# Performance work log

Measured on AMD Instinct MI355X. Metric: run time of the kernel, lower is better.

## Reference

```python
import jax, jax.numpy as jnp
import numpy as np

S, B, I, H, O = 1024, 64, 512, 2048, 512


def setup_inputs() -> dict:
    key = jax.random.key(0)
    k1, k2, k3, k4, k5 = jax.random.split(key, 5)
    X = jax.random.normal(k1, (S, B, I), dtype=jnp.float32)
    W_ih = jax.random.normal(k2, (H, I), dtype=jnp.float32) * (1.0 / np.sqrt(I))
    hh = jax.random.uniform(k3, (H,), dtype=jnp.float32)  # clamped-to-[-1,1] diagonal recurrence
    W_ho = jax.random.normal(k4, (O, H), dtype=jnp.float32) * (1.0 / np.sqrt(H))
    b_ho = jax.random.normal(k5, (O,), dtype=jnp.float32) * 0.01
    return {"X": X, "W_ih": W_ih, "hh": hh, "W_ho": W_ho, "b_ho": b_ho}


def reference(X, W_ih, hh, W_ho, b_ho):
    # Batch the input->hidden projection over the whole sequence in one GEMM:
    # u[s,b,h] = X[s,b,i] @ W_ih[h,i]^T
    u = jnp.einsum('sbi,hi->sbh', X, W_ih)
    h0 = jnp.zeros((X.shape[1], W_ih.shape[0]), dtype=X.dtype)

    def step(h, u_t):
        h_new = jnp.abs(u_t + hh * h)
        return h_new, None

    h_final, _ = jax.lax.scan(step, h0, u)
    Y = h_final @ W_ho.T + b_ho  # [B, O]
    return Y
```

## Files before the change

kernel.cpp:

```cpp
#include <hip/hip_runtime.h>
#include <hip/hip_bf16.h>
#include <stdint.h>

#define S_LEN 1024
#define B_SZ  64
#define I_SZ  512
#define H_SZ  2048
#define O_SZ  512

typedef __bf16  bf16x8 __attribute__((ext_vector_type(8)));
typedef float   f32x4  __attribute__((ext_vector_type(4)));

static __device__ __forceinline__ ushort f2bf(float f) {
  union { float f; unsigned u; } v; v.f = f;
  unsigned r = v.u + 0x7FFFu + ((v.u >> 16) & 1u);
  return (ushort)(r >> 16);
}
static __device__ __forceinline__ float bf2f(ushort u) {
  return __builtin_bit_cast(float, (unsigned)u << 16);
}

#define GLOAD_LDS16(gp, lp) \
  __builtin_amdgcn_global_load_lds( \
      (__attribute__((address_space(1))) void*)(gp), \
      (__attribute__((address_space(3))) void*)(lp), 16, 0, 0)

__global__ __launch_bounds__(256) void convert_f32_bf16_kernel(
    const float4* __restrict__ in, ushort4* __restrict__ out, int n4) {
  int i = blockIdx.x * 256 + threadIdx.x;
  if (i >= n4) return;
  float4 v = in[i];
  ushort4 o; o.x = f2bf(v.x); o.y = f2bf(v.y); o.z = f2bf(v.z); o.w = f2bf(v.w);
  out[i] = o;
}

__global__ __launch_bounds__(256) void convert_x_kernel(
    const float* __restrict__ X, ushort* __restrict__ Xt) {
  const int row  = blockIdx.x * 4 + (threadIdx.x >> 6);
  const int lane = threadIdx.x & 63;
  const int s = row >> 6, b = row & 63;
  const float* src = X + (size_t)row * I_SZ + lane * 8;
  float4 v0 = *(const float4*)src;
  float4 v1 = *(const float4*)(src + 4);
  union { ushort h[8]; uint4 v; } o;
  o.h[0] = f2bf(v0.x); o.h[1] = f2bf(v0.y); o.h[2] = f2bf(v0.z); o.h[3] = f2bf(v0.w);
  o.h[4] = f2bf(v1.x); o.h[5] = f2bf(v1.y); o.h[6] = f2bf(v1.z); o.h[7] = f2bf(v1.w);
  *(uint4*)(Xt + ((size_t)b * S_LEN + s) * I_SZ + lane * 8) = o.v;
}

__global__ __launch_bounds__(256) void init_y_kernel(
    const float* __restrict__ bho, float* __restrict__ Y) {
  int idx = blockIdx.x * 256 + threadIdx.x;
  Y[idx] = bho[idx & (O_SZ - 1)];
}

#define SCAN16(colp, s0_) do { \
    ushort4 v0 = *(const ushort4*)&(colp)[(s0_)]; \
    ushort4 v1 = *(const ushort4*)&(colp)[(s0_) + 4]; \
    ushort4 v2 = *(const ushort4*)&(colp)[(s0_) + 8]; \
    ushort4 v3 = *(const ushort4*)&(colp)[(s0_) + 12]; \
    p = fmaf(c, fabsf(p), bf2f(v0.x)); p = fmaf(c, fabsf(p), bf2f(v0.y)); \
    p = fmaf(c, fabsf(p), bf2f(v0.z)); p = fmaf(c, fabsf(p), bf2f(v0.w)); \
    p = fmaf(c, fabsf(p), bf2f(v1.x)); p = fmaf(c, fabsf(p), bf2f(v1.y)); \
    p = fmaf(c, fabsf(p), bf2f(v1.z)); p = fmaf(c, fabsf(p), bf2f(v1.w)); \
    p = fmaf(c, fabsf(p), bf2f(v2.x)); p = fmaf(c, fabsf(p), bf2f(v2.y)); \
    p = fmaf(c, fabsf(p), bf2f(v2.z)); p = fmaf(c, fabsf(p), bf2f(v2.w)); \
    p = fmaf(c, fabsf(p), bf2f(v3.x)); p = fmaf(c, fabsf(p), bf2f(v3.y)); \
    p = fmaf(c, fabsf(p), bf2f(v3.z)); p = fmaf(c, fabsf(p), bf2f(v3.w)); \
  } while (0)

__global__ __launch_bounds__(256, 3) void fused_gemm_scan_kernel(
    const ushort* __restrict__ Xbf,
    const ushort* __restrict__ Wbf,
    const float* __restrict__ hh,
    const float* __restrict__ Who,
    float* __restrict__ Y) {
  __shared__ __align__(16) ushort smem[16896];
  ushort* As = smem;
  ushort* Bs = smem + 8192;
  ushort* Cs = smem;

  const int tid  = threadIdx.x;
  const int wave = tid >> 6;
  const int lane = tid & 63;

  const int bid = blockIdx.x;
  const int xcd = bid & 7;
  const int g   = bid >> 3;
  const int b   = (xcd << 3) | (g & 7);
  const int ht  = g >> 3;

  const int wm = (wave >> 1) * 64;
  const int wn = (wave & 1) * 64;
  const int ml = lane & 15;
  const int q  = lane >> 4;

  const int r0     = wave * 32;
  const int srow   = lane >> 3;
  const int schunk = ((lane & 7) - srow) & 7;
  const ushort* gA = Xbf + (size_t)b * (S_LEN * I_SZ)
                   + (size_t)(r0 + srow) * I_SZ + schunk * 8;
  const ushort* gB = Wbf + (size_t)(ht * 128 + r0 + srow) * I_SZ + schunk * 8;
  ushort* lA = As + r0 * 64;
  ushort* lB = Bs + r0 * 64;

  int foff[2];
  foff[0] = ((q + ml) & 7) * 8;
  foff[1] = ((4 + q + ml) & 7) * 8;
  int arow[4], brow[4];
  #pragma unroll
  for (int i = 0; i < 4; ++i) {
    arow[i] = (wm + i * 16 + ml) * 64;
    brow[i] = (wn + i * 16 + ml) * 64;
  }

  float c = 0.0f, p = 0.0f;
  if (tid < 128) c = hh[ht * 128 + tid];

  #pragma unroll 1
  for (int st = 0; st < 8; ++st) {
    f32x4 acc[4][4] = {};

    for (int kt = 0; kt < 8; ++kt) {
      __syncthreads();
      const ushort* ga = gA + (size_t)st * (128 * I_SZ) + kt * 64;
      const ushort* gb = gB + kt * 64;
      #pragma unroll
      for (int jj = 0; jj < 4; ++jj) {
        GLOAD_LDS16(ga + (size_t)(jj * 8) * I_SZ, lA + jj * 512);
        GLOAD_LDS16(gb + (size_t)(jj * 8) * I_SZ, lB + jj * 512);
      }
      __syncthreads();
      #pragma unroll
      for (int ks = 0; ks < 2; ++ks) {
        bf16x8 af[4], bfr[4];
        #pragma unroll
        for (int i = 0; i < 4; ++i) {
          af[i]  = *(const bf16x8*)&As[arow[i] + foff[ks]];
          bfr[i] = *(const bf16x8*)&Bs[brow[i] + foff[ks]];
        }
        __builtin_amdgcn_s_setprio(1);
        #pragma unroll
        for (int mi = 0; mi < 4; ++mi)
          #pragma unroll
          for (int ni = 0; ni < 4; ++ni)
            acc[mi][ni] = __builtin_amdgcn_mfma_f32_16x16x32_bf16(
                af[mi], bfr[ni], acc[mi][ni], 0, 0, 0);
        __builtin_amdgcn_s_setprio(0);
      }
    }

    __syncthreads();
    const int sb = wm + q * 4;
    #pragma unroll
    for (int mi = 0; mi < 4; ++mi) {
      #pragma unroll
      for (int ni = 0; ni < 4; ++ni) {
        ushort4 o;
        o.x = f2bf(acc[mi][ni][0]); o.y = f2bf(acc[mi][ni][1]);
        o.z = f2bf(acc[mi][ni][2]); o.w = f2bf(acc[mi][ni][3]);
        *(ushort4*)&Cs[(wn + ni * 16 + ml) * 132 + sb + mi * 16] = o;
      }
    }
    __syncthreads();

    if (tid < 128) {
      const ushort* col = &Cs[tid * 132];
      #pragma unroll
      for (int s0 = 0; s0 < 128; s0 += 16) {
        SCAN16(col, s0);
      }
    }
  }

  __syncthreads();
  if (tid < 128) ((float*)smem)[tid] = fabsf(p);
  __syncthreads();

  {
    const float* hs = (const float*)smem;
    const float* w0 = Who + (size_t)tid * H_SZ + (size_t)ht * 128;
    const float* w1 = w0 + (size_t)256 * H_SZ;
    float y0 = 0.f, y1 = 0.f;
    #pragma unroll 8
    for (int k = 0; k < 128; k += 4) {
      float4 hv = *(const float4*)&hs[k];
      float4 u0 = *(const float4*)&w0[k];
      float4 u1 = *(const float4*)&w1[k];
      y0 += hv.x * u0.x + hv.y * u0.y + hv.z * u0.z + hv.w * u0.w;
      y1 += hv.x * u1.x + hv.y * u1.y + hv.z * u1.z + hv.w * u1.w;
    }
    atomicAdd(&Y[(size_t)b * O_SZ + tid], y0);
    atomicAdd(&Y[(size_t)b * O_SZ + 256 + tid], y1);
  }
}

extern "C" void kernel_launch(void* const* d_in, const int* in_sizes, int n_in,
                              void* d_out, int out_size, void* d_ws, size_t ws_size,
                              hipStream_t stream) {
  (void)in_sizes; (void)n_in; (void)out_size; (void)ws_size;
  const float* X   = (const float*)d_in[0];
  const float* Wih = (const float*)d_in[1];
  const float* hh  = (const float*)d_in[2];
  const float* Who = (const float*)d_in[3];
  const float* bho = (const float*)d_in[4];
  float* Y = (float*)d_out;

  const size_t WBF = (size_t)H_SZ * I_SZ * 2;
  char* w = (char*)d_ws;
  ushort* Wbf = (ushort*)w;
  ushort* Xbf = (ushort*)(w + WBF);

  {
    int n4w = (int)((size_t)H_SZ * I_SZ / 4);
    convert_f32_bf16_kernel<<<n4w / 256, 256, 0, stream>>>(
        (const float4*)Wih, (ushort4*)Wbf, n4w);
  }

  convert_x_kernel<<<(S_LEN * B_SZ) / 4, 256, 0, stream>>>(X, Xbf);

  init_y_kernel<<<(B_SZ * O_SZ) / 256, 256, 0, stream>>>(bho, Y);

  fused_gemm_scan_kernel<<<1024, 256, 0, stream>>>(Xbf, Wbf, hh, Who, Y);
}
```

Before: 413.3 us.

## Load GEMM fragments directly from global memory into registers, bypassing LDS staging

Removes the LDS staging of the X and W_ih tiles, which used global_load_lds plus two barriers per k-step. Each wave now loads its MFMA operand fragments straight from global memory into registers, and the k-loop is unrolled by two. The goals are to eliminate the barrier stalls and LDS traffic and to shrink shared memory so more blocks can be resident. In exchange, tiles shared across waves are fetched redundantly from global memory, through L2 and L1, and the loads are less coalesced, being 16-byte reads strided across rows.

Result: slower. 690.9 us (+67.2%).

```diff
diff --git a/kernel.cpp b/kernel.cpp
--- a/kernel.cpp
+++ b/kernel.cpp
@@ -19,11 +19,6 @@
 static __device__ __forceinline__ float bf2f(ushort u) {
   return __builtin_bit_cast(float, (unsigned)u << 16);
 }
-
-#define GLOAD_LDS16(gp, lp) \
-  __builtin_amdgcn_global_load_lds( \
-      (__attribute__((address_space(1))) void*)(gp), \
-      (__attribute__((address_space(3))) void*)(lp), 16, 0, 0)
 
 __global__ __launch_bounds__(256) void convert_f32_bf16_kernel(
     const float4* __restrict__ in, ushort4* __restrict__ out, int n4) {
@@ -75,10 +70,7 @@
     const float* __restrict__ hh,
     const float* __restrict__ Who,
     float* __restrict__ Y) {
-  __shared__ __align__(16) ushort smem[16896];
-  ushort* As = smem;
-  ushort* Bs = smem + 8192;
-  ushort* Cs = smem;
+  __shared__ __align__(16) ushort Cs[128 * 132];
 
   const int tid  = threadIdx.x;
   const int wave = tid >> 6;
@@ -95,24 +87,8 @@
   const int ml = lane & 15;
   const int q  = lane >> 4;
 
-  const int r0     = wave * 32;
-  const int srow   = lane >> 3;
-  const int schunk = ((lane & 7) - srow) & 7;
-  const ushort* gA = Xbf + (size_t)b * (S_LEN * I_SZ)
-                   + (size_t)(r0 + srow) * I_SZ + schunk * 8;
-  const ushort* gB = Wbf + (size_t)(ht * 128 + r0 + srow) * I_SZ + schunk * 8;
-  ushort* lA = As + r0 * 64;
-  ushort* lB = Bs + r0 * 64;
-
-  int foff[2];
-  foff[0] = ((q + ml) & 7) * 8;
-  foff[1] = ((4 + q + ml) & 7) * 8;
-  int arow[4], brow[4];
-  #pragma unroll
-  for (int i = 0; i < 4; ++i) {
-    arow[i] = (wm + i * 16 + ml) * 64;
-    brow[i] = (wn + i * 16 + ml) * 64;
-  }
+  const ushort* aBase = Xbf + ((size_t)b * S_LEN + wm + ml) * I_SZ + q * 8;
+  const ushort* bBase = Wbf + ((size_t)(ht * 128 + wn + ml)) * I_SZ + q * 8;
 
   float c = 0.0f, p = 0.0f;
   if (tid < 128) c = hh[ht * 128 + tid];
@@ -120,34 +96,35 @@
   #pragma unroll 1
   for (int st = 0; st < 8; ++st) {
     f32x4 acc[4][4] = {};
-
+    const ushort* aT = aBase + (size_t)st * (128 * I_SZ);
+
+    #pragma unroll 2
     for (int kt = 0; kt < 8; ++kt) {
-      __syncthreads();
-      const ushort* ga = gA + (size_t)st * (128 * I_SZ) + kt * 64;
-      const ushort* gb = gB + kt * 64;
-      #pragma unroll
-      for (int jj = 0; jj < 4; ++jj) {
-        GLOAD_LDS16(ga + (size_t)(jj * 8) * I_SZ, lA + jj * 512);
-        GLOAD_LDS16(gb + (size_t)(jj * 8) * I_SZ, lB + jj * 512);
+      const int ko = kt * 64;
+      bf16x8 a0[4], a1[4], b0[4], b1[4];
+      #pragma unroll
+      for (int i = 0; i < 4; ++i) {
+        const ushort* ap = aT + (size_t)(i * 16) * I_SZ + ko;
+        const ushort* bp = bBase + (size_t)(i * 16) * I_SZ + ko;
+        a0[i] = *(const bf16x8*)(ap);
+        a1[i] = *(const bf16x8*)(ap + 32);
+        b0[i] = *(const bf16x8*)(bp);
+        b1[i] = *(const bf16x8*)(bp + 32);
       }
-      __syncthreads();
-      #pragma unroll
-      for (int ks = 0; ks < 2; ++ks) {
-        bf16x8 af[4], bfr[4];
+      __builtin_amdgcn_s_setprio(1);
+      #pragma unroll
+      for (int mi = 0; mi < 4; ++mi)
         #pragma unroll
-        for (int i = 0; i < 4; ++i) {
-          af[i]  = *(const bf16x8*)&As[arow[i] + foff[ks]];
-          bfr[i] = *(const bf16x8*)&Bs[brow[i] + foff[ks]];
-        }
-        __builtin_amdgcn_s_setprio(1);
+        for (int ni = 0; ni < 4; ++ni)
+          acc[mi][ni] = __builtin_amdgcn_mfma_f32_16x16x32_bf16(
+              a0[mi], b0[ni], acc[mi][ni], 0, 0, 0);
+      #pragma unroll
+      for (int mi = 0; mi < 4; ++mi)
         #pragma unroll
-        for (int mi = 0; mi < 4; ++mi)
-          #pragma unroll
-          for (int ni = 0; ni < 4; ++ni)
-            acc[mi][ni] = __builtin_amdgcn_mfma_f32_16x16x32_bf16(
-                af[mi], bfr[ni], acc[mi][ni], 0, 0, 0);
-        __builtin_amdgcn_s_setprio(0);
-      }
+        for (int ni = 0; ni < 4; ++ni)
+          acc[mi][ni] = __builtin_amdgcn_mfma_f32_16x16x32_bf16(
+              a1[mi], b1[ni], acc[mi][ni], 0, 0, 0);
+      __builtin_amdgcn_s_setprio(0);
     }
 
     __syncthreads();
@@ -174,11 +151,11 @@
   }
 
   __syncthreads();
-  if (tid < 128) ((float*)smem)[tid] = fabsf(p);
+  if (tid < 128) ((float*)Cs)[tid] = fabsf(p);
   __syncthreads();
 
   {
-    const float* hs = (const float*)smem;
+    const float* hs = (const float*)Cs;
     const float* w0 = Who + (size_t)tid * H_SZ + (size_t)ht * 128;
     const float* w1 = w0 + (size_t)256 * H_SZ;
     float y0 = 0.f, y1 = 0.f;
```

## Prefetch next GEMM tile into registers while computing current tile

Applied to the files above, without the earlier changes.

Flattens the sequence-chunk and K loops into one 64-iteration loop. Each iteration issues global loads for the next A/B tile into registers before the MFMA work, then stores them to LDS after it, replacing the direct global-to-LDS loads that stalled before compute. The launch bound also rises from 3 to 4 blocks per CU. The register prefetch uses extra VGPRs and may fight the higher occupancy target, risking spills, and the scan still runs serially inside the loop.

After: 781.7 us. +89.2%, slower.

```diff
diff --git a/kernel.cpp b/kernel.cpp
--- a/kernel.cpp
+++ b/kernel.cpp
@@ -69,7 +69,7 @@
     p = fmaf(c, fabsf(p), bf2f(v3.z)); p = fmaf(c, fabsf(p), bf2f(v3.w)); \
   } while (0)
 
-__global__ __launch_bounds__(256, 3) void fused_gemm_scan_kernel(
+__global__ __launch_bounds__(256, 4) void fused_gemm_scan_kernel(
     const ushort* __restrict__ Xbf,
     const ushort* __restrict__ Wbf,
     const float* __restrict__ hh,
@@ -101,8 +101,10 @@
   const ushort* gA = Xbf + (size_t)b * (S_LEN * I_SZ)
                    + (size_t)(r0 + srow) * I_SZ + schunk * 8;
   const ushort* gB = Wbf + (size_t)(ht * 128 + r0 + srow) * I_SZ + schunk * 8;
-  ushort* lA = As + r0 * 64;
-  ushort* lB = Bs + r0 * 64;
+  ushort* lA = As + (r0 + srow) * 64 + (lane & 7) * 8;
+  ushort* lB = Bs + (r0 + srow) * 64 + (lane & 7) * 8;
+  ushort* pA = As + r0 * 64;
+  ushort* pB = Bs + r0 * 64;
 
   int foff[2];
   foff[0] = ((q + ml) & 7) * 8;
@@ -117,63 +119,93 @@
   float c = 0.0f, p = 0.0f;
   if (tid < 128) c = hh[ht * 128 + tid];
 
+  #pragma unroll
+  for (int jj = 0; jj < 4; ++jj) {
+    GLOAD_LDS16(gA + (size_t)(jj * 8) * I_SZ, pA + jj * 512);
+    GLOAD_LDS16(gB + (size_t)(jj * 8) * I_SZ, pB + jj * 512);
+  }
+  __syncthreads();
+
+  f32x4 acc[4][4];
+
   #pragma unroll 1
-  for (int st = 0; st < 8; ++st) {
-    f32x4 acc[4][4] = {};
-
-    for (int kt = 0; kt < 8; ++kt) {
+  for (int t = 0; t < 64; ++t) {
+    const int kt = t & 7;
+    if (kt == 0) {
+      #pragma unroll
+      for (int mi = 0; mi < 4; ++mi)
+        #pragma unroll
+        for (int ni = 0; ni < 4; ++ni) {
+          f32x4 z = {0.f, 0.f, 0.f, 0.f};
+          acc[mi][ni] = z;
+        }
+    }
+
+    uint4 rA[4], rB[4];
+    if (t < 63) {
+      const int n1 = t + 1;
+      const ushort* ga = gA + (size_t)(n1 >> 3) * (128 * I_SZ) + (n1 & 7) * 64;
+      const ushort* gb = gB + (size_t)(n1 & 7) * 64;
+      #pragma unroll
+      for (int jj = 0; jj < 4; ++jj) {
+        rA[jj] = *(const uint4*)(ga + (size_t)(jj * 8) * I_SZ);
+        rB[jj] = *(const uint4*)(gb + (size_t)(jj * 8) * I_SZ);
+      }
+    }
+
+    #pragma unroll
+    for (int ks = 0; ks < 2; ++ks) {
+      bf16x8 af[4], bfr[4];
+      #pragma unroll
+      for (int i = 0; i < 4; ++i) {
+        af[i]  = *(const bf16x8*)&As[arow[i] + foff[ks]];
+        bfr[i] = *(const bf16x8*)&Bs[brow[i] + foff[ks]];
+      }
+      __builtin_amdgcn_s_setprio(1);
+      #pragma unroll
+      for (int mi = 0; mi < 4; ++mi)
+        #pragma unroll
+        for (int ni = 0; ni < 4; ++ni)
+          acc[mi][ni] = __builtin_amdgcn_mfma_f32_16x16x32_bf16(
+              af[mi], bfr[ni], acc[mi][ni], 0, 0, 0);
+      __builtin_amdgcn_s_setprio(0);
+    }
+
+    __syncthreads();
+
+    if (kt == 7) {
+      const int sb = wm + q * 4;
+      #pragma unroll
+      for (int mi = 0; mi < 4; ++mi) {
+        #pragma unroll
+        for (int ni = 0; ni < 4; ++ni) {
+          ushort4 o;
+          o.x = f2bf(acc[mi][ni][0]); o.y = f2bf(acc[mi][ni][1]);
+          o.z = f2bf(acc[mi][ni][2]); o.w = f2bf(acc[mi][ni][3]);
+          *(ushort4*)&Cs[(wn + ni * 16 + ml) * 132 + sb + mi * 16] = o;
+        }
+      }
       __syncthreads();
-      const ushort* ga = gA + (size_t)st * (128 * I_SZ) + kt * 64;
-      const ushort* gb = gB + kt * 64;
+      if (tid < 128) {
+        const ushort* col = &Cs[tid * 132];
+        #pragma unroll
+        for (int s0 = 0; s0 < 128; s0 += 16) {
+          SCAN16(col, s0);
+        }
+      }
+      __syncthreads();
+    }
+
+    if (t < 63) {
       #pragma unroll
       for (int jj = 0; jj < 4; ++jj) {
-        GLOAD_LDS16(ga + (size_t)(jj * 8) * I_SZ, lA + jj * 512);
-        GLOAD_LDS16(gb + (size_t)(jj * 8) * I_SZ, lB + jj * 512);
+        *(uint4*)(lA + jj * 512) = rA[jj];
+        *(uint4*)(lB + jj * 512) = rB[jj];
       }
       __syncthreads();
-      #pragma unroll
-      for (int ks = 0; ks < 2; ++ks) {
-        bf16x8 af[4], bfr[4];
-        #pragma unroll
-        for (int i = 0; i < 4; ++i) {
-          af[i]  = *(const bf16x8*)&As[arow[i] + foff[ks]];
-          bfr[i] = *(const bf16x8*)&Bs[brow[i] + foff[ks]];
-        }
-        __builtin_amdgcn_s_setprio(1);
-        #pragma unroll
-        for (int mi = 0; mi < 4; ++mi)
-          #pragma unroll
-          for (int ni = 0; ni < 4; ++ni)
-            acc[mi][ni] = __builtin_amdgcn_mfma_f32_16x16x32_bf16(
-                af[mi], bfr[ni], acc[mi][ni], 0, 0, 0);
-        __builtin_amdgcn_s_setprio(0);
-      }
-    }
-
-    __syncthreads();
-    const int sb = wm + q * 4;
-    #pragma unroll
-    for (int mi = 0; mi < 4; ++mi) {
-      #pragma unroll
-      for (int ni = 0; ni < 4; ++ni) {
-        ushort4 o;
-        o.x = f2bf(acc[mi][ni][0]); o.y = f2bf(acc[mi][ni][1]);
-        o.z = f2bf(acc[mi][ni][2]); o.w = f2bf(acc[mi][ni][3]);
-        *(ushort4*)&Cs[(wn + ni * 16 + ml) * 132 + sb + mi * 16] = o;
-      }
-    }
-    __syncthreads();
-
-    if (tid < 128) {
-      const ushort* col = &Cs[tid * 132];
-      #pragma unroll
-      for (int s0 = 0; s0 < 128; s0 += 16) {
-        SCAN16(col, s0);
-      }
-    }
-  }
-
-  __syncthreads();
+    }
+  }
+
   if (tid < 128) ((float*)smem)[tid] = fabsf(p);
   __syncthreads();
 
```

## Double-buffer LDS tiles with K-step of 32 in a flattened GEMM-scan loop

Applied to the files above, without the earlier changes.

Replaces the two-barrier load-then-compute K loop with a single flattened loop over 128 steps of K=32. Each step prefetches the next A/B tile into a second LDS buffer while MFMAs consume the current one, with one barrier per step. The output staging tile moves to its own LDS region with a row stride of 130, so C writes no longer alias the operand buffers. The cost is roughly double the LDS per block and dropping the 3-blocks-per-CU launch hint, which may lower occupancy. The 130 stride also leaves the 8-byte C stores and scan reads misaligned on odd rows.

After: 476.8 us. 15.4% more time.

```diff
diff --git a/kernel.cpp b/kernel.cpp
--- a/kernel.cpp
+++ b/kernel.cpp
@@ -69,16 +69,23 @@
     p = fmaf(c, fabsf(p), bf2f(v3.z)); p = fmaf(c, fabsf(p), bf2f(v3.w)); \
   } while (0)
 
-__global__ __launch_bounds__(256, 3) void fused_gemm_scan_kernel(
+#define STAGE(dA, dB, T) do { \
+    const ushort* ga_ = gA + (size_t)((T) >> 4) * (128 * I_SZ) + ((T) & 15) * 32; \
+    const ushort* gb_ = gB + ((T) & 15) * 32; \
+    GLOAD_LDS16(ga_,              (dA) + stOff); \
+    GLOAD_LDS16(ga_ + 16 * I_SZ,  (dA) + stOff + 512); \
+    GLOAD_LDS16(gb_,              (dB) + stOff); \
+    GLOAD_LDS16(gb_ + 16 * I_SZ,  (dB) + stOff + 512); \
+  } while (0)
+
+__global__ __launch_bounds__(256) void fused_gemm_scan_kernel(
     const ushort* __restrict__ Xbf,
     const ushort* __restrict__ Wbf,
     const float* __restrict__ hh,
     const float* __restrict__ Who,
     float* __restrict__ Y) {
-  __shared__ __align__(16) ushort smem[16896];
-  ushort* As = smem;
-  ushort* Bs = smem + 8192;
-  ushort* Cs = smem;
+  __shared__ __align__(16) ushort smem[33024];
+  ushort* Cs = smem + 16384;
 
   const int tid  = threadIdx.x;
   const int wave = tid >> 6;
@@ -96,84 +103,91 @@
   const int q  = lane >> 4;
 
   const int r0     = wave * 32;
-  const int srow   = lane >> 3;
-  const int schunk = ((lane & 7) - srow) & 7;
+  const int lrow   = lane >> 2;
+  const int lchunk = ((lane & 3) - lrow) & 3;
   const ushort* gA = Xbf + (size_t)b * (S_LEN * I_SZ)
-                   + (size_t)(r0 + srow) * I_SZ + schunk * 8;
-  const ushort* gB = Wbf + (size_t)(ht * 128 + r0 + srow) * I_SZ + schunk * 8;
-  ushort* lA = As + r0 * 64;
-  ushort* lB = Bs + r0 * 64;
-
-  int foff[2];
-  foff[0] = ((q + ml) & 7) * 8;
-  foff[1] = ((4 + q + ml) & 7) * 8;
+                   + (size_t)(r0 + lrow) * I_SZ + lchunk * 8;
+  const ushort* gB = Wbf + (size_t)(ht * 128 + r0 + lrow) * I_SZ + lchunk * 8;
+  const int stOff = r0 * 32;
+
+  const int foff = ((q + ml) & 3) * 8;
   int arow[4], brow[4];
   #pragma unroll
   for (int i = 0; i < 4; ++i) {
-    arow[i] = (wm + i * 16 + ml) * 64;
-    brow[i] = (wn + i * 16 + ml) * 64;
+    arow[i] = (wm + i * 16 + ml) * 32;
+    brow[i] = (wn + i * 16 + ml) * 32;
   }
 
   float c = 0.0f, p = 0.0f;
   if (tid < 128) c = hh[ht * 128 + tid];
 
+  ushort* curA = smem;          ushort* curB = smem + 4096;
+  ushort* nxtA = smem + 8192;   ushort* nxtB = smem + 12288;
+
+  STAGE(curA, curB, 0);
+  __syncthreads();
+
+  f32x4 acc[4][4];
+
   #pragma unroll 1
-  for (int st = 0; st < 8; ++st) {
-    f32x4 acc[4][4] = {};
-
-    for (int kt = 0; kt < 8; ++kt) {
-      __syncthreads();
-      const ushort* ga = gA + (size_t)st * (128 * I_SZ) + kt * 64;
-      const ushort* gb = gB + kt * 64;
-      #pragma unroll
-      for (int jj = 0; jj < 4; ++jj) {
-        GLOAD_LDS16(ga + (size_t)(jj * 8) * I_SZ, lA + jj * 512);
-        GLOAD_LDS16(gb + (size_t)(jj * 8) * I_SZ, lB + jj * 512);
+  for (int t = 0; t < 128; ++t) {
+    if ((t & 15) == 0) {
+      #pragma unroll
+      for (int mi = 0; mi < 4; ++mi)
+        #pragma unroll
+        for (int ni = 0; ni < 4; ++ni) {
+          f32x4 z = {0.f, 0.f, 0.f, 0.f};
+          acc[mi][ni] = z;
+        }
+    }
+
+    if (t < 127) STAGE(nxtA, nxtB, t + 1);
+
+    {
+      bf16x8 af[4], bfr[4];
+      #pragma unroll
+      for (int i = 0; i < 4; ++i) {
+        af[i]  = *(const bf16x8*)&curA[arow[i] + foff];
+        bfr[i] = *(const bf16x8*)&curB[brow[i] + foff];
       }
-      __syncthreads();
-      #pragma unroll
-      for (int ks = 0; ks < 2; ++ks) {
-        bf16x8 af[4], bfr[4];
+      __builtin_amdgcn_s_setprio(1);
+      #pragma unroll
+      for (int mi = 0; mi < 4; ++mi)
         #pragma unroll
-        for (int i = 0; i < 4; ++i) {
-          af[i]  = *(const bf16x8*)&As[arow[i] + foff[ks]];
-          bfr[i] = *(const bf16x8*)&Bs[brow[i] + foff[ks]];
+        for (int ni = 0; ni < 4; ++ni)
+          acc[mi][ni] = __builtin_amdgcn_mfma_f32_16x16x32_bf16(
+              af[mi], bfr[ni], acc[mi][ni], 0, 0, 0);
+      __builtin_amdgcn_s_setprio(0);
+    }
+
+    if ((t & 15) == 15) {
+      const int sb = wm + q * 4;
+      #pragma unroll
+      for (int mi = 0; mi < 4; ++mi) {
+        #pragma unroll
+        for (int ni = 0; ni < 4; ++ni) {
+          ushort4 o;
+          o.x = f2bf(acc[mi][ni][0]); o.y = f2bf(acc[mi][ni][1]);
+          o.z = f2bf(acc[mi][ni][2]); o.w = f2bf(acc[mi][ni][3]);
+          *(ushort4*)&Cs[(wn + ni * 16 + ml) * 130 + sb + mi * 16] = o;
         }
-        __builtin_amdgcn_s_setprio(1);
-        #pragma unroll
-        for (int mi = 0; mi < 4; ++mi)
-          #pragma unroll
-          for (int ni = 0; ni < 4; ++ni)
-            acc[mi][ni] = __builtin_amdgcn_mfma_f32_16x16x32_bf16(
-                af[mi], bfr[ni], acc[mi][ni], 0, 0, 0);
-        __builtin_amdgcn_s_setprio(0);
       }
     }
 
     __syncthreads();
-    const int sb = wm + q * 4;
-    #pragma unroll
-    for (int mi = 0; mi < 4; ++mi) {
-      #pragma unroll
-      for (int ni = 0; ni < 4; ++ni) {
-        ushort4 o;
-        o.x = f2bf(acc[mi][ni][0]); o.y = f2bf(acc[mi][ni][1]);
-        o.z = f2bf(acc[mi][ni][2]); o.w = f2bf(acc[mi][ni][3]);
-        *(ushort4*)&Cs[(wn + ni * 16 + ml) * 132 + sb + mi * 16] = o;
-      }
-    }
-    __syncthreads();
-
-    if (tid < 128) {
-      const ushort* col = &Cs[tid * 132];
+
+    if ((t & 15) == 15 && tid < 128) {
+      const ushort* col = &Cs[tid * 130];
       #pragma unroll
       for (int s0 = 0; s0 < 128; s0 += 16) {
         SCAN16(col, s0);
       }
     }
-  }
-
-  __syncthreads();
+
+    ushort* tA = curA; curA = nxtA; nxtA = tA;
+    ushort* tB = curB; curB = nxtB; nxtB = tB;
+  }
+
   if (tid < 128) ((float*)smem)[tid] = fabsf(p);
   __syncthreads();
 
```
